# Optimization experiments

Hardware: AMD Instinct MI355X
Metric: run time of the kernel (lower is better)

## Reference

```python
import jax, jax.numpy as jnp
import numpy as np
from jax import lax

INPUT_DIM = 256
STATE_DIM = 512
B, T = 128, 1024


def setup_inputs() -> dict:
    key = jax.random.key(0)
    ks = jax.random.split(key, 9)
    s = STATE_DIM
    i = INPUT_DIM
    # Linear(state_dim, state_dim, bias=False), weight scaled by 0.2 as in __init__
    lim_s = 1.0 / np.sqrt(s)
    lim_i = 1.0 / np.sqrt(i)
    A0_w = jax.random.uniform(ks[0], (s, s), jnp.float32, -lim_s, lim_s) * 0.2
    A1_w = jax.random.uniform(ks[1], (s, s), jnp.float32, -lim_s, lim_s) * 0.2
    B0_w = jax.random.uniform(ks[2], (s, i), jnp.float32, -lim_i, lim_i)
    B0_b = jax.random.uniform(ks[3], (s,), jnp.float32, -lim_i, lim_i)
    B1_w = jax.random.uniform(ks[4], (s, i), jnp.float32, -lim_i, lim_i)
    B1_b = jax.random.uniform(ks[5], (s,), jnp.float32, -lim_i, lim_i)
    gate_w = jax.random.uniform(ks[6], (s, i), jnp.float32, -lim_i, lim_i)
    gate_b = jax.random.uniform(ks[7], (s,), jnp.float32, -lim_i, lim_i)
    x_seq = jax.random.normal(ks[8], (B, T, i), jnp.float32)
    s0 = jnp.zeros((B, s), jnp.float32)
    alpha = jnp.float32(0.5)
    return {
        "x_seq": x_seq, "s0": s0,
        "A0_w": A0_w, "B0_w": B0_w, "B0_b": B0_b,
        "A1_w": A1_w, "B1_w": B1_w, "B1_b": B1_b,
        "gate_w": gate_w, "gate_b": gate_b,
        "alpha": alpha, "z": 1,
    }


def reference(x_seq, s0, A0_w, B0_w, B0_b, A1_w, B1_w, B1_b, gate_w, gate_b, alpha, z):
    # Precompute all input projections in one batched GEMM each: [B, T, S]
    bx0 = jnp.einsum('bti,si->bts', x_seq, B0_w) + B0_b
    bx1 = jnp.einsum('bti,si->bts', x_seq, B1_w) + B1_b
    gx = jax.nn.sigmoid(jnp.einsum('bti,si->bts', x_seq, gate_w) + gate_b)

    def step_fn(s, inputs):
        b0_t, b1_t, g_t = inputs  # each [B, S]
        f0 = jnp.tanh(s @ A0_w.T + b0_t)
        if z == 0:
            f = f0
        else:
            f1 = jnp.tanh(s @ A1_w.T + b1_t)
            f = (1.0 - alpha) * f0 + alpha * f1
        s_new = g_t * f + (1.0 - g_t) * s
        return s_new, s_new

    # scan over time: move T to leading axis
    xs = (jnp.swapaxes(bx0, 0, 1), jnp.swapaxes(bx1, 0, 1), jnp.swapaxes(gx, 0, 1))
    _, states = lax.scan(step_fn, s0, xs)  # states: [T, B, S]
    # prepend s0 -> [B, T+1, S]
    return jnp.concatenate([s0[:, None, :], jnp.swapaxes(states, 0, 1)], axis=1)
```

## Files before the change

### kernel.cpp

```cpp
#include <hip/hip_runtime.h>
#include <hip/hip_bf16.h>
#include <math.h>

typedef __attribute__((ext_vector_type(8))) short bf16x8;
typedef __attribute__((ext_vector_type(4))) float f32x4;
typedef __attribute__((ext_vector_type(4))) int i32x4;

#define TT 1024
#define BB 128
#define II 256
#define SS 512
#define OUT_T 1025
#define OUT_BSTRIDE ((size_t)OUT_T * SS)

static __device__ __forceinline__ unsigned short f2bf(float f) {
  union { float f; unsigned int u; } v; v.f = f;
  unsigned int r = v.u + 0x7fffu + ((v.u >> 16) & 1u);
  return (unsigned short)(r >> 16);
}
static __device__ __forceinline__ float bf2f(unsigned short h) {
  union { unsigned int u; float f; } v; v.u = ((unsigned int)h) << 16;
  return v.f;
}
static __device__ __forceinline__ bf16x8 pack8(const float* p) {
  float4 a = *(const float4*)p;
  float4 b = *(const float4*)(p + 4);
  bf16x8 r;
  r[0]=(short)f2bf(a.x); r[1]=(short)f2bf(a.y); r[2]=(short)f2bf(a.z); r[3]=(short)f2bf(a.w);
  r[4]=(short)f2bf(b.x); r[5]=(short)f2bf(b.y); r[6]=(short)f2bf(b.z); r[7]=(short)f2bf(b.w);
  return r;
}
static __device__ __forceinline__ float fast_tanh(float x) {
  float x2 = fminf(x * 2.8853900817779268f, 88.0f);
  float e = __builtin_amdgcn_exp2f(x2);
  return (e - 1.0f) * __builtin_amdgcn_rcpf(e + 1.0f);
}

static __device__ __forceinline__ i32x4 ld_coh_b128_issue(const void* p) {
  i32x4 r;
  asm volatile("global_load_dwordx4 %0, %1, off sc0 sc1" : "=v"(r) : "v"(p) : "memory");
  return r;
}
static __device__ __forceinline__ unsigned int ld_coh_b32(const void* p) {
  unsigned int r;
  asm volatile("global_load_dword %0, %1, off sc0 sc1\n\ts_waitcnt vmcnt(0)"
               : "=v"(r) : "v"(p) : "memory");
  return r;
}
static __device__ __forceinline__ void st_coh_b128(void* p, i32x4 v) {
  asm volatile("global_store_dwordx4 %0, %1, off sc0 sc1" :: "v"(p), "v"(v) : "memory");
}
static __device__ __forceinline__ void st_coh_b32(void* p, unsigned int v) {
  asm volatile("global_store_dword %0, %1, off sc0 sc1" :: "v"(p), "v"(v) : "memory");
}
static __device__ __forceinline__ void waitcnt_vm0() {
  asm volatile("s_waitcnt vmcnt(0)" ::: "memory");
}

__global__ __launch_bounds__(256) void proj_kernel(
    const float* __restrict__ x,
    const float* __restrict__ B0w, const float* __restrict__ B0b,
    const float* __restrict__ B1w, const float* __restrict__ B1b,
    const float* __restrict__ Gw,  const float* __restrict__ Gb,
    unsigned short* __restrict__ proj)
{
  __shared__ unsigned short Ab[64 * 40];
  __shared__ unsigned short Bb[64 * 40];
  int bid = blockIdx.x;
  int nb = bid % 24, mb = bid / 24;
  int m0 = mb * 64, n0 = nb * 64;
  const float* Wp; const float* bp; bool isgate = false;
  if (n0 < 512)       { Wp = B0w + (size_t)n0 * II;          bp = B0b + n0; }
  else if (n0 < 1024) { Wp = B1w + (size_t)(n0 - 512) * II;  bp = B1b + (n0 - 512); }
  else                { Wp = Gw  + (size_t)(n0 - 1024) * II; bp = Gb + (n0 - 1024); isgate = true; }

  int tid = threadIdx.x;
  int lane = tid & 63, wid = tid >> 6;
  int r = tid >> 2, c = tid & 3;
  int mt0 = (wid >> 1) * 2, nt0 = (wid & 1) * 2;

  f32x4 acc[2][2] = {};
  for (int k0 = 0; k0 < II; k0 += 32) {
    __syncthreads();
    *(bf16x8*)&Ab[r * 40 + c * 8] = pack8(x  + (size_t)(m0 + r) * II + k0 + c * 8);
    *(bf16x8*)&Bb[r * 40 + c * 8] = pack8(Wp + (size_t)r * II       + k0 + c * 8);
    __syncthreads();
    bf16x8 af[2], bf[2];
#pragma unroll
    for (int mi = 0; mi < 2; ++mi)
      af[mi] = *(const bf16x8*)&Ab[((mt0 + mi) * 16 + (lane & 15)) * 40 + 8 * (lane >> 4)];
#pragma unroll
    for (int ni = 0; ni < 2; ++ni)
      bf[ni] = *(const bf16x8*)&Bb[((nt0 + ni) * 16 + (lane & 15)) * 40 + 8 * (lane >> 4)];
#pragma unroll
    for (int mi = 0; mi < 2; ++mi)
#pragma unroll
      for (int ni = 0; ni < 2; ++ni)
        acc[mi][ni] = __builtin_amdgcn_mfma_f32_16x16x32_bf16(af[mi], bf[ni], acc[mi][ni], 0, 0, 0);
  }
#pragma unroll
  for (int mi = 0; mi < 2; ++mi)
#pragma unroll
    for (int ni = 0; ni < 2; ++ni)
#pragma unroll
      for (int q = 0; q < 4; ++q) {
        int m  = m0 + (mt0 + mi) * 16 + (lane >> 4) * 4 + q;
        int nl = (nt0 + ni) * 16 + (lane & 15);
        int b = m >> 10, t = m & 1023;
        float v = acc[mi][ni][q] + bp[nl];
        if (isgate) v = 1.0f / (1.0f + expf(-v));
        proj[((size_t)t * BB + b) * 1536 + n0 + nl] = f2bf(v);
      }
}

__global__ __launch_bounds__(256, 1) void recur_kernel(
    const float* __restrict__ s0,
    const float* __restrict__ A0w, const float* __restrict__ A1w,
    const unsigned short* __restrict__ proj,
    const float* __restrict__ alpha_p, const int* __restrict__ z_p,
    unsigned short* state_bf,
    unsigned int* flags,
    float* __restrict__ out)
{
  __shared__ unsigned short Ss[16 * 520];

  int tid = threadIdx.x, lane = tid & 63, wid = tid >> 6;
  int g = blockIdx.x & 7, j = blockIdx.x >> 3;
  int b0 = g * 16, c0 = j * 64;
  int lane15 = lane & 15, kslot = lane >> 4;
  int rowbase = kslot * 4;
  int colw = c0 + wid * 16 + lane15;
  float alpha = *alpha_p; int z = *z_p;
  float om_a = 1.0f - alpha;

  bf16x8 Af0[16], Af1[16];
#pragma unroll
  for (int kk = 0; kk < 16; ++kk) {
    int k0 = kk * 32 + kslot * 8;
    Af0[kk] = pack8(A0w + (size_t)colw * SS + k0);
    Af1[kk] = pack8(A1w + (size_t)colw * SS + k0);
  }

#pragma unroll
  for (int c2 = 0; c2 < 4; ++c2) {
    int e = tid + 256 * c2; int rr = e >> 6, kc = e & 63;
    *(bf16x8*)&Ss[rr * 520 + kc * 8] = pack8(s0 + (size_t)(b0 + rr) * SS + kc * 8);
  }
  if (j == 0) {
#pragma unroll
    for (int c2 = 0; c2 < 4; ++c2) {
      int e = tid + 256 * c2; int rr = e >> 6, kc = e & 63;
      const float* sp = s0 + (size_t)(b0 + rr) * SS + kc * 8;
      float* op = out + (size_t)(b0 + rr) * OUT_BSTRIDE + kc * 8;
      *(float4*)op = *(const float4*)sp;
      *(float4*)(op + 4) = *(const float4*)(sp + 4);
    }
  }
  float sprev[4];
#pragma unroll
  for (int q = 0; q < 4; ++q)
    sprev[q] = s0[(size_t)(b0 + rowbase + q) * SS + colw];

  const unsigned short* pj[4];
  unsigned short pb0[4], pb1[4], pg[4];
#pragma unroll
  for (int q = 0; q < 4; ++q) {
    pj[q] = proj + (size_t)(b0 + rowbase + q) * 1536 + colw;
    pb0[q] = pj[q][0]; pb1[q] = pj[q][512]; pg[q] = pj[q][1024];
  }

  __syncthreads();

  for (int t = 0; t < TT; ++t) {
    f32x4 acc0 = {0.f,0.f,0.f,0.f}, acc1 = {0.f,0.f,0.f,0.f};
    const unsigned short* sb = &Ss[lane15 * 520 + kslot * 8];
#pragma unroll
    for (int kk = 0; kk < 16; ++kk) {
      bf16x8 af = *(const bf16x8*)(sb + kk * 32);
      acc0 = __builtin_amdgcn_mfma_f32_16x16x32_bf16(af, Af0[kk], acc0, 0, 0, 0);
      acc1 = __builtin_amdgcn_mfma_f32_16x16x32_bf16(af, Af1[kk], acc1, 0, 0, 0);
    }
    __syncthreads();

    float sn[4];
#pragma unroll
    for (int q = 0; q < 4; ++q) {
      float f0 = fast_tanh(acc0[q] + bf2f(pb0[q]));
      float f;
      if (z != 0) {
        float f1 = fast_tanh(acc1[q] + bf2f(pb1[q]));
        f = om_a * f0 + alpha * f1;
      } else {
        f = f0;
      }
      float gg = bf2f(pg[q]);
      sn[q] = gg * f + (1.0f - gg) * sprev[q];
      sprev[q] = sn[q];
      Ss[(rowbase + q) * 520 + colw] = f2bf(sn[q]);
    }
    __syncthreads();

    unsigned short* snext = state_bf + (size_t)((t + 1) & 1) * BB * SS;
    if (tid < 128) {
      int row = tid >> 3, ch = tid & 7;
      i32x4 v = *(const i32x4*)&Ss[row * 520 + c0 + ch * 8];
      st_coh_b128(snext + (size_t)(b0 + row) * SS + c0 + ch * 8, v);
      waitcnt_vm0();
    }
    __syncthreads();
    if (tid == 0) st_coh_b32(flags + g * 8 + j, (unsigned int)(t + 1));

#pragma unroll
    for (int q = 0; q < 4; ++q)
      out[(size_t)(b0 + rowbase + q) * OUT_BSTRIDE + (size_t)(t + 1) * SS + colw] = sn[q];
    if (t + 1 < TT) {
#pragma unroll
      for (int q = 0; q < 4; ++q) {
        pj[q] += (size_t)BB * 1536;
        pb0[q] = pj[q][0]; pb1[q] = pj[q][512]; pg[q] = pj[q][1024];
      }
      if (wid == 0 && lane < 8) {
        const unsigned int* fp = flags + g * 8 + lane;
        while (ld_coh_b32(fp) < (unsigned int)(t + 1)) {}
      }
      __syncthreads();
      i32x4 v[4];
#pragma unroll
      for (int c2 = 0; c2 < 4; ++c2) {
        int e = tid + 256 * c2; int rr = e >> 6, kc = e & 63;
        v[c2] = ld_coh_b128_issue(snext + (size_t)(b0 + rr) * SS + kc * 8);
      }
      waitcnt_vm0();
#pragma unroll
      for (int c2 = 0; c2 < 4; ++c2) {
        int e = tid + 256 * c2; int rr = e >> 6, kc = e & 63;
        *(bf16x8*)&Ss[rr * 520 + kc * 8] = *(bf16x8*)&v[c2];
      }
      __syncthreads();
    }
  }
}

extern "C" void kernel_launch(void* const* d_in, const int* in_sizes, int n_in,
                              void* d_out, int out_size, void* d_ws, size_t ws_size,
                              hipStream_t stream) {
  const float* x   = (const float*)d_in[0];
  const float* s0  = (const float*)d_in[1];
  const float* A0w = (const float*)d_in[2];
  const float* B0w = (const float*)d_in[3];
  const float* B0b = (const float*)d_in[4];
  const float* A1w = (const float*)d_in[5];
  const float* B1w = (const float*)d_in[6];
  const float* B1b = (const float*)d_in[7];
  const float* Gw  = (const float*)d_in[8];
  const float* Gb  = (const float*)d_in[9];
  const float* alp = (const float*)d_in[10];
  const int*   zp  = (const int*)d_in[11];
  float* out = (float*)d_out;

  char* ws = (char*)d_ws;
  size_t proj_bytes  = (size_t)BB * TT * 1536 * 2;
  size_t state_off   = proj_bytes;
  size_t state_bytes = (size_t)2 * BB * SS * 2;
  size_t flag_off    = state_off + state_bytes;
  unsigned short* proj     = (unsigned short*)(ws);
  unsigned short* state_bf = (unsigned short*)(ws + state_off);
  unsigned int*   flags    = (unsigned int*)(ws + flag_off);

  hipMemsetAsync(flags, 0, 64 * sizeof(unsigned int), stream);

  proj_kernel<<<dim3((131072 / 64) * (1536 / 64)), dim3(256), 0, stream>>>(
      x, B0w, B0b, B1w, B1b, Gw, Gb, proj);

  recur_kernel<<<dim3(64), dim3(256), 0, stream>>>(
      s0, A0w, A1w, proj, alp, zp, state_bf, flags, out);
}
```

Before: 3.026 ms.

## Halve recurrence blocks, overlap peer-state loads with local MFMA, restage projection tiles

The recurrence kernel now runs 32 blocks, each owning 128 state columns, so each 16-row group syncs with 4 peers instead of 8. Each step first runs the MFMAs on the block's own state slice while the three peer slices load, then finishes with the remote slices. This hides global-load latency and removes one barrier round. The projection kernel now stages a whole 64-row x tile in LDS once and loops over all 24 output tiles, cutting redundant x reads at the cost of fewer, heavier blocks and more weight registers per thread in the recurrence.

```diff
diff --git a/kernel.cpp b/kernel.cpp
--- a/kernel.cpp
+++ b/kernel.cpp
@@ -64,53 +64,61 @@
     const float* __restrict__ Gw,  const float* __restrict__ Gb,
     unsigned short* __restrict__ proj)
 {
-  __shared__ unsigned short Ab[64 * 40];
-  __shared__ unsigned short Bb[64 * 40];
-  int bid = blockIdx.x;
-  int nb = bid % 24, mb = bid / 24;
-  int m0 = mb * 64, n0 = nb * 64;
-  const float* Wp; const float* bp; bool isgate = false;
-  if (n0 < 512)       { Wp = B0w + (size_t)n0 * II;          bp = B0b + n0; }
-  else if (n0 < 1024) { Wp = B1w + (size_t)(n0 - 512) * II;  bp = B1b + (n0 - 512); }
-  else                { Wp = Gw  + (size_t)(n0 - 1024) * II; bp = Gb + (n0 - 1024); isgate = true; }
-
-  int tid = threadIdx.x;
-  int lane = tid & 63, wid = tid >> 6;
-  int r = tid >> 2, c = tid & 3;
+  __shared__ unsigned short Xs[64 * 264];
+  __shared__ unsigned short Ws[64 * 40];
+
+  int m0 = blockIdx.x * 64;
+  int tid = threadIdx.x, lane = tid & 63, wid = tid >> 6;
+  int lane15 = lane & 15, kslot = lane >> 4;
   int mt0 = (wid >> 1) * 2, nt0 = (wid & 1) * 2;
-
-  f32x4 acc[2][2] = {};
-  for (int k0 = 0; k0 < II; k0 += 32) {
-    __syncthreads();
-    *(bf16x8*)&Ab[r * 40 + c * 8] = pack8(x  + (size_t)(m0 + r) * II + k0 + c * 8);
-    *(bf16x8*)&Bb[r * 40 + c * 8] = pack8(Wp + (size_t)r * II       + k0 + c * 8);
-    __syncthreads();
-    bf16x8 af[2], bf[2];
+  int sr = tid >> 2, sc = tid & 3;
+
+#pragma unroll
+  for (int it = 0; it < 8; ++it) {
+    int task = tid + 256 * it; int r = task >> 5, c = task & 31;
+    *(bf16x8*)&Xs[r * 264 + c * 8] = pack8(x + (size_t)(m0 + r) * II + c * 8);
+  }
+  __syncthreads();
+
+  for (int nt = 0; nt < 24; ++nt) {
+    int n0 = nt * 64;
+    const float* Wp; const float* bp; bool isgate = false;
+    if (n0 < 512)       { Wp = B0w + (size_t)n0 * II;          bp = B0b + n0; }
+    else if (n0 < 1024) { Wp = B1w + (size_t)(n0 - 512) * II;  bp = B1b + (n0 - 512); }
+    else                { Wp = Gw  + (size_t)(n0 - 1024) * II; bp = Gb + (n0 - 1024); isgate = true; }
+
+    f32x4 acc[2][2] = {};
+    for (int k0 = 0; k0 < II; k0 += 32) {
+      __syncthreads();
+      *(bf16x8*)&Ws[sr * 40 + sc * 8] = pack8(Wp + (size_t)sr * II + k0 + sc * 8);
+      __syncthreads();
+      bf16x8 af[2], bf[2];
+#pragma unroll
+      for (int mi = 0; mi < 2; ++mi)
+        af[mi] = *(const bf16x8*)&Xs[((mt0 + mi) * 16 + lane15) * 264 + k0 + 8 * kslot];
+#pragma unroll
+      for (int ni = 0; ni < 2; ++ni)
+        bf[ni] = *(const bf16x8*)&Ws[((nt0 + ni) * 16 + lane15) * 40 + 8 * kslot];
+#pragma unroll
+      for (int mi = 0; mi < 2; ++mi)
+#pragma unroll
+        for (int ni = 0; ni < 2; ++ni)
+          acc[mi][ni] = __builtin_amdgcn_mfma_f32_16x16x32_bf16(af[mi], bf[ni], acc[mi][ni], 0, 0, 0);
+    }
 #pragma unroll
     for (int mi = 0; mi < 2; ++mi)
-      af[mi] = *(const bf16x8*)&Ab[((mt0 + mi) * 16 + (lane & 15)) * 40 + 8 * (lane >> 4)];
-#pragma unroll
-    for (int ni = 0; ni < 2; ++ni)
-      bf[ni] = *(const bf16x8*)&Bb[((nt0 + ni) * 16 + (lane & 15)) * 40 + 8 * (lane >> 4)];
-#pragma unroll
-    for (int mi = 0; mi < 2; ++mi)
 #pragma unroll
       for (int ni = 0; ni < 2; ++ni)
-        acc[mi][ni] = __builtin_amdgcn_mfma_f32_16x16x32_bf16(af[mi], bf[ni], acc[mi][ni], 0, 0, 0);
-  }
-#pragma unroll
-  for (int mi = 0; mi < 2; ++mi)
-#pragma unroll
-    for (int ni = 0; ni < 2; ++ni)
-#pragma unroll
-      for (int q = 0; q < 4; ++q) {
-        int m  = m0 + (mt0 + mi) * 16 + (lane >> 4) * 4 + q;
-        int nl = (nt0 + ni) * 16 + (lane & 15);
-        int b = m >> 10, t = m & 1023;
-        float v = acc[mi][ni][q] + bp[nl];
-        if (isgate) v = 1.0f / (1.0f + expf(-v));
-        proj[((size_t)t * BB + b) * 1536 + n0 + nl] = f2bf(v);
-      }
+#pragma unroll
+        for (int q = 0; q < 4; ++q) {
+          int m  = m0 + (mt0 + mi) * 16 + kslot * 4 + q;
+          int nl = (nt0 + ni) * 16 + lane15;
+          int b = m >> 10, t = m & 1023;
+          float v = acc[mi][ni][q] + bp[nl];
+          if (isgate) v = 1.0f / (1.0f + expf(-v));
+          proj[((size_t)t * BB + b) * 1536 + n0 + nl] = f2bf(v);
+        }
+  }
 }
 
 __global__ __launch_bounds__(256, 1) void recur_kernel(
@@ -126,19 +134,21 @@
 
   int tid = threadIdx.x, lane = tid & 63, wid = tid >> 6;
   int g = blockIdx.x & 7, j = blockIdx.x >> 3;
-  int b0 = g * 16, c0 = j * 64;
+  int b0 = g * 16, c0 = j * 128;
   int lane15 = lane & 15, kslot = lane >> 4;
   int rowbase = kslot * 4;
-  int colw = c0 + wid * 16 + lane15;
-  float alpha = *alpha_p; int z = *z_p;
-  float om_a = 1.0f - alpha;
-
-  bf16x8 Af0[16], Af1[16];
+  int colt0 = c0 + wid * 32 + lane15;
+  int colt1 = colt0 + 16;
+  float alpha = *alpha_p; int z = *z_p; float om_a = 1.0f - alpha;
+
+  bf16x8 Bf0[2][16], Bf1[2][16];
 #pragma unroll
   for (int kk = 0; kk < 16; ++kk) {
     int k0 = kk * 32 + kslot * 8;
-    Af0[kk] = pack8(A0w + (size_t)colw * SS + k0);
-    Af1[kk] = pack8(A1w + (size_t)colw * SS + k0);
+    Bf0[0][kk] = pack8(A0w + (size_t)colt0 * SS + k0);
+    Bf0[1][kk] = pack8(A0w + (size_t)colt1 * SS + k0);
+    Bf1[0][kk] = pack8(A1w + (size_t)colt0 * SS + k0);
+    Bf1[1][kk] = pack8(A1w + (size_t)colt1 * SS + k0);
   }
 
 #pragma unroll
@@ -148,95 +158,133 @@
   }
   if (j == 0) {
 #pragma unroll
-    for (int c2 = 0; c2 < 4; ++c2) {
-      int e = tid + 256 * c2; int rr = e >> 6, kc = e & 63;
-      const float* sp = s0 + (size_t)(b0 + rr) * SS + kc * 8;
-      float* op = out + (size_t)(b0 + rr) * OUT_BSTRIDE + kc * 8;
-      *(float4*)op = *(const float4*)sp;
-      *(float4*)(op + 4) = *(const float4*)(sp + 4);
-    }
-  }
-  float sprev[4];
-#pragma unroll
-  for (int q = 0; q < 4; ++q)
-    sprev[q] = s0[(size_t)(b0 + rowbase + q) * SS + colw];
-
+    for (int it = 0; it < 8; ++it) {
+      int task = tid + 256 * it;
+      int rr = task >> 7, f4 = task & 127;
+      *(float4*)(out + (size_t)(b0 + rr) * OUT_BSTRIDE + f4 * 4) =
+          *(const float4*)(s0 + (size_t)(b0 + rr) * SS + f4 * 4);
+    }
+  }
+  float sprev[2][4];
+#pragma unroll
+  for (int q = 0; q < 4; ++q) {
+    sprev[0][q] = s0[(size_t)(b0 + rowbase + q) * SS + colt0];
+    sprev[1][q] = s0[(size_t)(b0 + rowbase + q) * SS + colt1];
+  }
   const unsigned short* pj[4];
-  unsigned short pb0[4], pb1[4], pg[4];
+  unsigned short pb0[2][4], pb1[2][4], pg[2][4];
 #pragma unroll
   for (int q = 0; q < 4; ++q) {
-    pj[q] = proj + (size_t)(b0 + rowbase + q) * 1536 + colw;
-    pb0[q] = pj[q][0]; pb1[q] = pj[q][512]; pg[q] = pj[q][1024];
-  }
-
+    pj[q] = proj + (size_t)(b0 + rowbase + q) * 1536;
+#pragma unroll
+    for (int ct = 0; ct < 2; ++ct) {
+      int cc = (ct == 0) ? colt0 : colt1;
+      pb0[ct][q] = pj[q][cc]; pb1[ct][q] = pj[q][cc + 512]; pg[ct][q] = pj[q][cc + 1024];
+    }
+  }
+
+  int prow = tid >> 4, pch = tid & 15;
   __syncthreads();
 
   for (int t = 0; t < TT; ++t) {
-    f32x4 acc0 = {0.f,0.f,0.f,0.f}, acc1 = {0.f,0.f,0.f,0.f};
+    f32x4 acc0[2] = {}, acc1[2] = {};
     const unsigned short* sb = &Ss[lane15 * 520 + kslot * 8];
-#pragma unroll
-    for (int kk = 0; kk < 16; ++kk) {
-      bf16x8 af = *(const bf16x8*)(sb + kk * 32);
-      acc0 = __builtin_amdgcn_mfma_f32_16x16x32_bf16(af, Af0[kk], acc0, 0, 0, 0);
-      acc1 = __builtin_amdgcn_mfma_f32_16x16x32_bf16(af, Af1[kk], acc1, 0, 0, 0);
+
+    if (t == 0) {
+#pragma unroll
+      for (int kk = 0; kk < 16; ++kk) {
+        bf16x8 af = *(const bf16x8*)(sb + kk * 32);
+        acc0[0] = __builtin_amdgcn_mfma_f32_16x16x32_bf16(af, Bf0[0][kk], acc0[0], 0, 0, 0);
+        acc0[1] = __builtin_amdgcn_mfma_f32_16x16x32_bf16(af, Bf0[1][kk], acc0[1], 0, 0, 0);
+        acc1[0] = __builtin_amdgcn_mfma_f32_16x16x32_bf16(af, Bf1[0][kk], acc1[0], 0, 0, 0);
+        acc1[1] = __builtin_amdgcn_mfma_f32_16x16x32_bf16(af, Bf1[1][kk], acc1[1], 0, 0, 0);
+      }
+    } else {
+      const unsigned short* sbt = state_bf + (size_t)(t & 1) * BB * SS;
+      i32x4 pv[3];
+#pragma unroll
+      for (int idx = 1; idx < 4; ++idx) {
+        int p = (j + idx) & 3;
+        while (ld_coh_b32(flags + g * 4 + p) < (unsigned int)t) {}
+        pv[idx - 1] = ld_coh_b128_issue(sbt + (size_t)(b0 + prow) * SS + p * 128 + pch * 8);
+      }
+#pragma unroll
+      for (int kk2 = 0; kk2 < 4; ++kk2) {
+        int kk = j * 4 + kk2;
+        bf16x8 af = *(const bf16x8*)(sb + kk * 32);
+        acc0[0] = __builtin_amdgcn_mfma_f32_16x16x32_bf16(af, Bf0[0][kk], acc0[0], 0, 0, 0);
+        acc0[1] = __builtin_amdgcn_mfma_f32_16x16x32_bf16(af, Bf0[1][kk], acc0[1], 0, 0, 0);
+        acc1[0] = __builtin_amdgcn_mfma_f32_16x16x32_bf16(af, Bf1[0][kk], acc1[0], 0, 0, 0);
+        acc1[1] = __builtin_amdgcn_mfma_f32_16x16x32_bf16(af, Bf1[1][kk], acc1[1], 0, 0, 0);
+      }
+      waitcnt_vm0();
+#pragma unroll
+      for (int idx = 1; idx < 4; ++idx) {
+        int p = (j + idx) & 3;
+        *(bf16x8*)&Ss[prow * 520 + p * 128 + pch * 8] = *(bf16x8*)&pv[idx - 1];
+      }
+      __syncthreads();
+#pragma unroll
+      for (int idx = 1; idx < 4; ++idx) {
+        int p = (j + idx) & 3;
+#pragma unroll
+        for (int kk2 = 0; kk2 < 4; ++kk2) {
+          int kk = p * 4 + kk2;
+          bf16x8 af = *(const bf16x8*)(sb + kk * 32);
+          acc0[0] = __builtin_amdgcn_mfma_f32_16x16x32_bf16(af, Bf0[0][kk], acc0[0], 0, 0, 0);
+          acc0[1] = __builtin_amdgcn_mfma_f32_16x16x32_bf16(af, Bf0[1][kk], acc0[1], 0, 0, 0);
+          acc1[0] = __builtin_amdgcn_mfma_f32_16x16x32_bf16(af, Bf1[0][kk], acc1[0], 0, 0, 0);
+          acc1[1] = __builtin_amdgcn_mfma_f32_16x16x32_bf16(af, Bf1[1][kk], acc1[1], 0, 0, 0);
+        }
+      }
+    }
+
+    float sn[2][4];
+#pragma unroll
+    for (int ct = 0; ct < 2; ++ct) {
+      int cc = (ct == 0) ? colt0 : colt1;
+#pragma unroll
+      for (int q = 0; q < 4; ++q) {
+        float f0 = fast_tanh(acc0[ct][q] + bf2f(pb0[ct][q]));
+        float f;
+        if (z != 0) {
+          float f1 = fast_tanh(acc1[ct][q] + bf2f(pb1[ct][q]));
+          f = om_a * f0 + alpha * f1;
+        } else f = f0;
+        float gg = bf2f(pg[ct][q]);
+        sn[ct][q] = gg * f + (1.0f - gg) * sprev[ct][q];
+        sprev[ct][q] = sn[ct][q];
+        Ss[(rowbase + q) * 520 + cc] = f2bf(sn[ct][q]);
+      }
     }
     __syncthreads();
 
-    float sn[4];
-#pragma unroll
-    for (int q = 0; q < 4; ++q) {
-      float f0 = fast_tanh(acc0[q] + bf2f(pb0[q]));
-      float f;
-      if (z != 0) {
-        float f1 = fast_tanh(acc1[q] + bf2f(pb1[q]));
-        f = om_a * f0 + alpha * f1;
-      } else {
-        f = f0;
-      }
-      float gg = bf2f(pg[q]);
-      sn[q] = gg * f + (1.0f - gg) * sprev[q];
-      sprev[q] = sn[q];
-      Ss[(rowbase + q) * 520 + colw] = f2bf(sn[q]);
+    unsigned short* snx = state_bf + (size_t)((t + 1) & 1) * BB * SS;
+    {
+      i32x4 v = *(const i32x4*)&Ss[prow * 520 + c0 + pch * 8];
+      st_coh_b128(snx + (size_t)(b0 + prow) * SS + c0 + pch * 8, v);
+      waitcnt_vm0();
     }
     __syncthreads();
-
-    unsigned short* snext = state_bf + (size_t)((t + 1) & 1) * BB * SS;
-    if (tid < 128) {
-      int row = tid >> 3, ch = tid & 7;
-      i32x4 v = *(const i32x4*)&Ss[row * 520 + c0 + ch * 8];
-      st_coh_b128(snext + (size_t)(b0 + row) * SS + c0 + ch * 8, v);
-      waitcnt_vm0();
-    }
-    __syncthreads();
-    if (tid == 0) st_coh_b32(flags + g * 8 + j, (unsigned int)(t + 1));
-
-#pragma unroll
-    for (int q = 0; q < 4; ++q)
-      out[(size_t)(b0 + rowbase + q) * OUT_BSTRIDE + (size_t)(t + 1) * SS + colw] = sn[q];
+    if (tid == 0) st_coh_b32(flags + g * 4 + j, (unsigned int)(t + 1));
+
+#pragma unroll
+    for (int ct = 0; ct < 2; ++ct) {
+      int cc = (ct == 0) ? colt0 : colt1;
+#pragma unroll
+      for (int q = 0; q < 4; ++q)
+        out[(size_t)(b0 + rowbase + q) * OUT_BSTRIDE + (size_t)(t + 1) * SS + cc] = sn[ct][q];
+    }
     if (t + 1 < TT) {
 #pragma unroll
       for (int q = 0; q < 4; ++q) {
         pj[q] += (size_t)BB * 1536;
-        pb0[q] = pj[q][0]; pb1[q] = pj[q][512]; pg[q] = pj[q][1024];
-      }
-      if (wid == 0 && lane < 8) {
-        const unsigned int* fp = flags + g * 8 + lane;
-        while (ld_coh_b32(fp) < (unsigned int)(t + 1)) {}
-      }
-      __syncthreads();
-      i32x4 v[4];
-#pragma unroll
-      for (int c2 = 0; c2 < 4; ++c2) {
-        int e = tid + 256 * c2; int rr = e >> 6, kc = e & 63;
-        v[c2] = ld_coh_b128_issue(snext + (size_t)(b0 + rr) * SS + kc * 8);
-      }
-      waitcnt_vm0();
-#pragma unroll
-      for (int c2 = 0; c2 < 4; ++c2) {
-        int e = tid + 256 * c2; int rr = e >> 6, kc = e & 63;
-        *(bf16x8*)&Ss[rr * 520 + kc * 8] = *(bf16x8*)&v[c2];
-      }
-      __syncthreads();
+#pragma unroll
+        for (int ct = 0; ct < 2; ++ct) {
+          int cc = (ct == 0) ? colt0 : colt1;
+          pb0[ct][q] = pj[q][cc]; pb1[ct][q] = pj[q][cc + 512]; pg[ct][q] = pj[q][cc + 1024];
+        }
+      }
     }
   }
 }
@@ -269,9 +317,9 @@
 
   hipMemsetAsync(flags, 0, 64 * sizeof(unsigned int), stream);
 
-  proj_kernel<<<dim3((131072 / 64) * (1536 / 64)), dim3(256), 0, stream>>>(
+  proj_kernel<<<dim3(131072 / 64), dim3(256), 0, stream>>>(
       x, B0w, B0b, B1w, B1b, Gw, Gb, proj);
 
-  recur_kernel<<<dim3(64), dim3(256), 0, stream>>>(
+  recur_kernel<<<dim3(32), dim3(256), 0, stream>>>(
       s0, A0w, A1w, proj, alp, zp, state_bf, flags, out);
 }
```

After: 10.37 ms. +242.5%, slower.
